# Kernel optimization log

Hardware: AMD Instinct MI355X
Metric: run time of the kernel (lower is better)

Reference implementation:

```python
import jax, jax.numpy as jnp
import numpy as np
from jax import lax

ALPHA = 0.1
B, C_IN, T, D_MODEL = 32, 512, 2048, 1024


def setup_inputs() -> dict:
    key = jax.random.key(0)
    k_x, k_w, k_b = jax.random.split(key, 3)
    x = jax.random.normal(k_x, (B, C_IN, T), dtype=jnp.float32)
    # nn.Linear(c_in, d_model): weight [d_model, c_in], bias [d_model]
    bound = 1.0 / np.sqrt(C_IN)
    W = jax.random.uniform(k_w, (D_MODEL, C_IN), dtype=jnp.float32, minval=-bound, maxval=bound)
    b = jax.random.uniform(k_b, (D_MODEL,), dtype=jnp.float32, minval=-bound, maxval=bound)
    return {"x": x, "W": W, "b": b}


def _ewma_scan(xt):
    # xt: [T, B, C] time-major; f_0 = x_0, f_t = a*x_t + (1-a)*f_{t-1}
    def step(carry, xi):
        carry = ALPHA * xi + (1.0 - ALPHA) * carry
        return carry, carry
    _, ys = lax.scan(step, xt[0], xt[1:])
    return jnp.concatenate([xt[:1], ys], axis=0)  # [T, B, C]


def reference(x, W, b):
    # x: [B, c_in, T] -> permute to [B, T, c_in]
    xp = jnp.transpose(x, (0, 2, 1))
    xt = jnp.moveaxis(xp, 1, 0)  # [T, B, c_in]
    fwd = _ewma_scan(xt)
    bwd = _ewma_scan(xt[::-1])[::-1]
    ewma = jnp.moveaxis((fwd + bwd) * 0.5, 0, 1)  # [B, T, c_in]
    # value embedding (dropout = identity at inference)
    return jnp.einsum('btc,dc->btd', ewma, W) + b
```

## Files before the change

### kernel.cpp

```cpp
#include <hip/hip_runtime.h>
#include <hip/hip_bf16.h>
#include <stdint.h>
#include <stddef.h>

#define T_LEN   2048
#define C_IN_   512
#define D_MODEL_ 1024
#define B_SZ    32

typedef __hip_bfloat16 bf16;
typedef __attribute__((ext_vector_type(8))) short short8;
typedef __attribute__((ext_vector_type(4))) float f32x4;

__device__ __forceinline__ void gload16(const void* g, void* l) {
    __builtin_amdgcn_global_load_lds(
        (const __attribute__((address_space(1))) uint32_t*)g,
        (__attribute__((address_space(3))) uint32_t*)l, 16, 0, 0);
}

__global__ void wconv_kernel(const float* __restrict__ W, bf16* __restrict__ Wb) {
    int i = blockIdx.x * 256 + threadIdx.x;
    float4 v = ((const float4*)W)[i];
    bf16* o = Wb + (size_t)i * 4;
    o[0] = __float2bfloat16(v.x);
    o[1] = __float2bfloat16(v.y);
    o[2] = __float2bfloat16(v.z);
    o[3] = __float2bfloat16(v.w);
}

__global__ __launch_bounds__(512)
void ewma_kernel(const float* __restrict__ x, bf16* __restrict__ A) {
    const int tid  = threadIdx.x;
    const int wid  = tid >> 6;
    const int lane = tid & 63;
    const int half = lane >> 5;
    const int j    = lane & 31;
    const int b    = blockIdx.x >> 5;
    const int cg   = blockIdx.x & 31;
    const int c_local = (wid << 1) | half;
    const int c    = (cg << 4) + c_local;

    const float AL = 0.1f, OM = 0.9f;
    const float Q  = 1.179018457773862e-3f;

    float xr[64];
    const float4* xp = (const float4*)(x + (size_t)(b * C_IN_ + c) * T_LEN + j * 64);
    #pragma unroll
    for (int i = 0; i < 16; ++i) {
        float4 v = xp[i];
        xr[4*i+0] = v.x; xr[4*i+1] = v.y; xr[4*i+2] = v.z; xr[4*i+3] = v.w;
    }

    float g = (j == 0) ? xr[0] : AL * xr[0];
    #pragma unroll
    for (int i = 1; i < 64; ++i) g = fmaf(OM, g, AL * xr[i]);

    float F = g, coef = Q;
    #pragma unroll
    for (int d = 1; d < 32; d <<= 1) {
        float up = __shfl_up(F, d, 32);
        F += (j >= d) ? coef * up : 0.0f;
        coef *= coef;
    }
    float carry = __shfl_up(F, 1, 32);
    if (j == 0) carry = 0.0f;

    xr[0] = (j == 0) ? xr[0] : fmaf(OM, carry, AL * xr[0]);
    #pragma unroll
    for (int i = 1; i < 64; ++i) xr[i] = fmaf(OM, xr[i-1], AL * xr[i]);

    float h;
    {
        float incL = xr[63] - OM * xr[62];
        if (j == 31) incL *= 10.0f;
        h = incL;
        #pragma unroll
        for (int i = 62; i >= 1; --i) h = fmaf(OM, h, xr[i] - OM * xr[i-1]);
        float inc0 = (j == 0) ? AL * xr[0] : (xr[0] - OM * carry);
        h = fmaf(OM, h, inc0);
    }

    float Bv = h; coef = Q;
    #pragma unroll
    for (int d = 1; d < 32; d <<= 1) {
        float dn = __shfl_down(Bv, d, 32);
        Bv += (j < 32 - d) ? coef * dn : 0.0f;
        coef *= coef;
    }
    float bnext = __shfl_down(Bv, 1, 32);
    if (j == 31) bnext = 0.0f;

    {
        float bp = bnext;
        float incL = xr[63] - OM * xr[62];
        if (j == 31) incL *= 10.0f;
        float bb = fmaf(OM, bp, incL);
        xr[63] = 0.5f * (xr[63] + bb);
        bp = bb;
        #pragma unroll
        for (int i = 62; i >= 1; --i) {
            float inc = xr[i] - OM * xr[i-1];
            bb = fmaf(OM, bp, inc);
            xr[i] = 0.5f * (xr[i] + bb);
            bp = bb;
        }
        float inc0 = (j == 0) ? AL * xr[0] : (xr[0] - OM * carry);
        bb = fmaf(OM, bp, inc0);
        xr[0] = 0.5f * (xr[0] + bb);
    }

    __shared__ bf16 stg[32 * 16 * 16];
    const size_t outbase = (size_t)(b * T_LEN) * C_IN_ + (cg << 4);
    #pragma unroll
    for (int grp = 0; grp < 4; ++grp) {
        __syncthreads();
        #pragma unroll
        for (int ii = 0; ii < 16; ++ii) {
            int elem = ((j * 16 + ii) * 16 + c_local) ^ ((j & 7) << 3);
            stg[elem] = __float2bfloat16(xr[grp * 16 + ii]);
        }
        __syncthreads();
        #pragma unroll
        for (int r = 0; r < 2; ++r) {
            int u   = tid * 2 + r;
            int jj  = u >> 5;
            int ii  = (u >> 1) & 15;
            int hf  = u & 1;
            int elem = ((jj * 16 + ii) * 16 + hf * 8) ^ ((jj & 7) << 3);
            float4 v = *(const float4*)&stg[elem];
            int t = jj * 64 + grp * 16 + ii;
            *(float4*)(A + outbase + (size_t)t * C_IN_ + hf * 8) = v;
        }
    }
}

#define MFMA(a, b, c) __builtin_amdgcn_mfma_f32_16x16x32_bf16(a, b, c, 0, 0, 0)

__global__ __launch_bounds__(512)
void gemm_kernel(const bf16* __restrict__ Amat, const bf16* __restrict__ Wb,
                 const float* __restrict__ bias, float* __restrict__ out) {
    constexpr int K = C_IN_, N = D_MODEL_;
    extern __shared__ bf16 lds[];
    const int tid  = threadIdx.x;
    const int wid  = tid >> 6, lane = tid & 63;
    const int wr   = wid >> 2, wc = wid & 3;
    const int lr   = lane & 15;
    const int lg   = lane >> 4;

    int bid = blockIdx.x;
    int swz = (bid & 7) * 128 + (bid >> 3);
    const int mb = swz >> 2, nb = swz & 3;
    const int m0 = mb * 256, n0 = nb * 256;

    auto base = [&](int s, int op, int hf) -> bf16* {
        return lds + (((s * 2 + op) * 2 + hf) << 13);
    };
    auto stage = [&](const bf16* g, int row0, int kt, int s, int op, int hf) {
        bf16* lb = base(s, op, hf);
        #pragma unroll
        for (int r = 0; r < 2; ++r) {
            int q = tid + r * 512;
            int row = q >> 3, u = q & 7;
            gload16(g + (size_t)(row0 + row) * K + kt * 64 + ((u ^ (row & 7)) << 3),
                    (char*)lb + q * 16);
        }
    };
    auto rdA = [&](int s, int mf, int ks) -> short8 {
        int row = mf * 16 + lr;
        int u   = ks * 4 + lg;
        return *(const short8*)((const char*)base(s, 0, wr)
                                + row * 128 + ((u ^ (row & 7)) << 4));
    };
    auto rdB = [&](int s, int nf, int ks) -> short8 {
        int row = (wc & 1) * 64 + nf * 16 + lr;
        int u   = ks * 4 + lg;
        return *(const short8*)((const char*)base(s, 1, wc >> 1)
                                + row * 128 + ((u ^ (row & 7)) << 4));
    };

    f32x4 acc[8][4];
    #pragma unroll
    for (int m = 0; m < 8; ++m)
        #pragma unroll
        for (int n = 0; n < 4; ++n) acc[m][n] = (f32x4){0.f, 0.f, 0.f, 0.f};

    stage(Amat, m0 + 0,   0, 0, 0, 0);
    stage(Amat, m0 + 128, 0, 0, 0, 1);
    stage(Wb,   n0 + 0,   0, 0, 1, 0);
    stage(Wb,   n0 + 128, 0, 0, 1, 1);
    stage(Amat, m0 + 0,   1, 1, 0, 0);
    asm volatile("s_waitcnt vmcnt(2)" ::: "memory");
    __builtin_amdgcn_s_barrier();

    #pragma unroll
    for (int kt = 0; kt < 8; ++kt) {
        const int s = kt & 1;
        short8 a[4][2], bA[2][2], bB[2][2];

        #pragma unroll
        for (int m = 0; m < 4; ++m) { a[m][0] = rdA(s, m, 0); a[m][1] = rdA(s, m, 1); }
        #pragma unroll
        for (int n = 0; n < 2; ++n) { bA[n][0] = rdB(s, n, 0); bA[n][1] = rdB(s, n, 1); }
        if (kt < 7) stage(Amat, m0 + 128, kt + 1, s ^ 1, 0, 1);
        __builtin_amdgcn_s_barrier();
        asm volatile("s_waitcnt lgkmcnt(0)");
        __builtin_amdgcn_sched_barrier(0);
        __builtin_amdgcn_s_setprio(1);
        #pragma unroll
        for (int m = 0; m < 4; ++m)
            #pragma unroll
            for (int n = 0; n < 2; ++n) {
                acc[m][n] = MFMA(a[m][0], bA[n][0], acc[m][n]);
                acc[m][n] = MFMA(a[m][1], bA[n][1], acc[m][n]);
            }
        __builtin_amdgcn_s_setprio(0);
        __builtin_amdgcn_s_barrier();

        #pragma unroll
        for (int n = 0; n < 2; ++n) { bB[n][0] = rdB(s, 2 + n, 0); bB[n][1] = rdB(s, 2 + n, 1); }
        if (kt < 7) stage(Wb, n0 + 0, kt + 1, s ^ 1, 1, 0);
        __builtin_amdgcn_s_barrier();
        asm volatile("s_waitcnt lgkmcnt(0)");
        __builtin_amdgcn_sched_barrier(0);
        __builtin_amdgcn_s_setprio(1);
        #pragma unroll
        for (int m = 0; m < 4; ++m)
            #pragma unroll
            for (int n = 0; n < 2; ++n) {
                acc[m][2 + n] = MFMA(a[m][0], bB[n][0], acc[m][2 + n]);
                acc[m][2 + n] = MFMA(a[m][1], bB[n][1], acc[m][2 + n]);
            }
        __builtin_amdgcn_s_setprio(0);
        __builtin_amdgcn_s_barrier();

        #pragma unroll
        for (int m = 0; m < 4; ++m) { a[m][0] = rdA(s, 4 + m, 0); a[m][1] = rdA(s, 4 + m, 1); }
        if (kt < 7) stage(Wb, n0 + 128, kt + 1, s ^ 1, 1, 1);
        __builtin_amdgcn_s_barrier();
        asm volatile("s_waitcnt lgkmcnt(0)");
        __builtin_amdgcn_sched_barrier(0);
        __builtin_amdgcn_s_setprio(1);
        #pragma unroll
        for (int m = 0; m < 4; ++m)
            #pragma unroll
            for (int n = 0; n < 2; ++n) {
                acc[4 + m][2 + n] = MFMA(a[m][0], bB[n][0], acc[4 + m][2 + n]);
                acc[4 + m][2 + n] = MFMA(a[m][1], bB[n][1], acc[4 + m][2 + n]);
            }
        __builtin_amdgcn_s_setprio(0);
        __builtin_amdgcn_s_barrier();

        if (kt < 6) stage(Amat, m0 + 0, kt + 2, s, 0, 0);
        __builtin_amdgcn_s_setprio(1);
        #pragma unroll
        for (int m = 0; m < 4; ++m)
            #pragma unroll
            for (int n = 0; n < 2; ++n) {
                acc[4 + m][n] = MFMA(a[m][0], bA[n][0], acc[4 + m][n]);
                acc[4 + m][n] = MFMA(a[m][1], bA[n][1], acc[4 + m][n]);
            }
        __builtin_amdgcn_s_setprio(0);
        if (kt < 6)       asm volatile("s_waitcnt vmcnt(2)" ::: "memory");
        else if (kt == 6) asm volatile("s_waitcnt vmcnt(0)" ::: "memory");
        __builtin_amdgcn_s_barrier();
    }

    const int crow = (lane >> 4) << 2;
    #pragma unroll
    for (int nf = 0; nf < 4; ++nf) {
        int col = n0 + wc * 64 + nf * 16 + lr;
        float bv = bias[col];
        #pragma unroll
        for (int mf = 0; mf < 8; ++mf) {
            size_t rbase = (size_t)(m0 + wr * 128 + mf * 16 + crow) * N + col;
            #pragma unroll
            for (int r = 0; r < 4; ++r)
                out[rbase + (size_t)r * N] = acc[mf][nf][r] + bv;
        }
    }
}

extern "C" void kernel_launch(void* const* d_in, const int* in_sizes, int n_in,
                              void* d_out, int out_size, void* d_ws, size_t ws_size,
                              hipStream_t stream) {
    const float* x    = (const float*)d_in[0];
    const float* W    = (const float*)d_in[1];
    const float* bias = (const float*)d_in[2];
    float* out = (float*)d_out;

    bf16* Wb   = (bf16*)d_ws;
    bf16* Amat = (bf16*)((char*)d_ws + (1 << 21));

    hipLaunchKernelGGL(wconv_kernel, dim3(512), dim3(256), 0, stream, W, Wb);
    hipLaunchKernelGGL(ewma_kernel, dim3(B_SZ * 32), dim3(512), 0, stream, x, Amat);
    hipLaunchKernelGGL(gemm_kernel,
                       dim3((B_SZ * T_LEN / 256) * (D_MODEL_ / 256)),
                       dim3(512), 131072, stream, Amat, Wb, bias, out);
}
```

Measured before the change: 172.6 us.

## Coalesce EWMA input loads through LDS and deepen GEMM prefetch schedule

The EWMA kernel now stages each block's 16 channel rows through shared memory with asynchronous global-to-LDS loads and a swizzle, instead of having each thread read its 64-element strided chunk directly. This targets coalescing of the input reads, at the cost of 64KB of LDS per block and extra barriers. The GEMM main loop is unrolled by two k-steps with a reordered staging sequence that keeps more loads in flight (vmcnt(4) instead of vmcnt(2)). It also drops the sched_barrier hints, which aims to hide global-load latency better but leaves instruction ordering to the compiler.

```diff
diff --git a/kernel.cpp b/kernel.cpp
--- a/kernel.cpp
+++ b/kernel.cpp
@@ -38,17 +38,36 @@
     const int b    = blockIdx.x >> 5;
     const int cg   = blockIdx.x & 31;
     const int c_local = (wid << 1) | half;
-    const int c    = (cg << 4) + c_local;
 
     const float AL = 0.1f, OM = 0.9f;
     const float Q  = 1.179018457773862e-3f;
 
+    __shared__ float buf[8 * 2048];
+    __shared__ bf16  stg[32 * 16 * 16];
+
     float xr[64];
-    const float4* xp = (const float4*)(x + (size_t)(b * C_IN_ + c) * T_LEN + j * 64);
-    #pragma unroll
-    for (int i = 0; i < 16; ++i) {
-        float4 v = xp[i];
-        xr[4*i+0] = v.x; xr[4*i+1] = v.y; xr[4*i+2] = v.z; xr[4*i+3] = v.w;
+    const size_t xbase = ((size_t)b * C_IN_ + (cg << 4)) * T_LEN;
+    const int srcu = tid ^ ((tid >> 4) & 7);
+
+    #pragma unroll
+    for (int h = 0; h < 2; ++h) {
+        #pragma unroll
+        for (int it = 0; it < 8; ++it)
+            gload16(x + xbase + (size_t)(h * 8 + it) * T_LEN + srcu * 4,
+                    (char*)buf + it * 8192 + tid * 16);
+        asm volatile("s_waitcnt vmcnt(0)" ::: "memory");
+        __syncthreads();
+        if ((c_local >> 3) == h) {
+            const char* rbase = (const char*)buf + (c_local & 7) * 8192;
+            #pragma unroll
+            for (int i = 0; i < 16; ++i) {
+                int p = (j * 16 + i) ^ (j & 7);
+                float4 v = *(const float4*)(rbase + p * 16);
+                xr[4*i+0] = v.x; xr[4*i+1] = v.y;
+                xr[4*i+2] = v.z; xr[4*i+3] = v.w;
+            }
+        }
+        __syncthreads();
     }
 
     float g = (j == 0) ? xr[0] : AL * xr[0];
@@ -69,18 +88,18 @@
     #pragma unroll
     for (int i = 1; i < 64; ++i) xr[i] = fmaf(OM, xr[i-1], AL * xr[i]);
 
-    float h;
+    float h2;
     {
         float incL = xr[63] - OM * xr[62];
         if (j == 31) incL *= 10.0f;
-        h = incL;
-        #pragma unroll
-        for (int i = 62; i >= 1; --i) h = fmaf(OM, h, xr[i] - OM * xr[i-1]);
+        h2 = incL;
+        #pragma unroll
+        for (int i = 62; i >= 1; --i) h2 = fmaf(OM, h2, xr[i] - OM * xr[i-1]);
         float inc0 = (j == 0) ? AL * xr[0] : (xr[0] - OM * carry);
-        h = fmaf(OM, h, inc0);
-    }
-
-    float Bv = h; coef = Q;
+        h2 = fmaf(OM, h2, inc0);
+    }
+
+    float Bv = h2; coef = Q;
     #pragma unroll
     for (int d = 1; d < 32; d <<= 1) {
         float dn = __shfl_down(Bv, d, 32);
@@ -109,7 +128,6 @@
         xr[0] = 0.5f * (xr[0] + bb);
     }
 
-    __shared__ bf16 stg[32 * 16 * 16];
     const size_t outbase = (size_t)(b * T_LEN) * C_IN_ + (cg << 4);
     #pragma unroll
     for (int grp = 0; grp < 4; ++grp) {
@@ -155,27 +173,27 @@
     auto base = [&](int s, int op, int hf) -> bf16* {
         return lds + (((s * 2 + op) * 2 + hf) << 13);
     };
-    auto stage = [&](const bf16* g, int row0, int kt, int s, int op, int hf) {
+    auto stageH = [&](int op, int hf, int kt, int s) {
+        const bf16* g = (op == 0) ? Amat + (size_t)(m0 + hf * 128) * K
+                                  : Wb   + (size_t)(n0 + hf * 128) * K;
         bf16* lb = base(s, op, hf);
         #pragma unroll
         for (int r = 0; r < 2; ++r) {
             int q = tid + r * 512;
             int row = q >> 3, u = q & 7;
-            gload16(g + (size_t)(row0 + row) * K + kt * 64 + ((u ^ (row & 7)) << 3),
+            gload16(g + (size_t)row * K + kt * 64 + ((u ^ (row & 7)) << 3),
                     (char*)lb + q * 16);
         }
     };
     auto rdA = [&](int s, int mf, int ks) -> short8 {
         int row = mf * 16 + lr;
-        int u   = ks * 4 + lg;
         return *(const short8*)((const char*)base(s, 0, wr)
-                                + row * 128 + ((u ^ (row & 7)) << 4));
+                                + row * 128 + (((ks * 4 + lg) ^ (row & 7)) << 4));
     };
     auto rdB = [&](int s, int nf, int ks) -> short8 {
         int row = (wc & 1) * 64 + nf * 16 + lr;
-        int u   = ks * 4 + lg;
         return *(const short8*)((const char*)base(s, 1, wc >> 1)
-                                + row * 128 + ((u ^ (row & 7)) << 4));
+                                + row * 128 + (((ks * 4 + lg) ^ (row & 7)) << 4));
     };
 
     f32x4 acc[8][4];
@@ -184,27 +202,23 @@
         #pragma unroll
         for (int n = 0; n < 4; ++n) acc[m][n] = (f32x4){0.f, 0.f, 0.f, 0.f};
 
-    stage(Amat, m0 + 0,   0, 0, 0, 0);
-    stage(Amat, m0 + 128, 0, 0, 0, 1);
-    stage(Wb,   n0 + 0,   0, 0, 1, 0);
-    stage(Wb,   n0 + 128, 0, 0, 1, 1);
-    stage(Amat, m0 + 0,   1, 1, 0, 0);
-    asm volatile("s_waitcnt vmcnt(2)" ::: "memory");
+    stageH(0, 0, 0, 0); stageH(0, 1, 0, 0); stageH(1, 0, 0, 0); stageH(1, 1, 0, 0);
+    stageH(1, 0, 1, 1); stageH(0, 0, 1, 1);
+    asm volatile("s_waitcnt vmcnt(4)" ::: "memory");
     __builtin_amdgcn_s_barrier();
 
     #pragma unroll
-    for (int kt = 0; kt < 8; ++kt) {
-        const int s = kt & 1;
+    for (int it = 0; it < 4; ++it) {
+        const int k0 = 2 * it;
         short8 a[4][2], bA[2][2], bB[2][2];
 
         #pragma unroll
-        for (int m = 0; m < 4; ++m) { a[m][0] = rdA(s, m, 0); a[m][1] = rdA(s, m, 1); }
-        #pragma unroll
-        for (int n = 0; n < 2; ++n) { bA[n][0] = rdB(s, n, 0); bA[n][1] = rdB(s, n, 1); }
-        if (kt < 7) stage(Amat, m0 + 128, kt + 1, s ^ 1, 0, 1);
-        __builtin_amdgcn_s_barrier();
-        asm volatile("s_waitcnt lgkmcnt(0)");
-        __builtin_amdgcn_sched_barrier(0);
+        for (int m = 0; m < 4; ++m) { a[m][0] = rdA(0, m, 0); a[m][1] = rdA(0, m, 1); }
+        #pragma unroll
+        for (int n = 0; n < 2; ++n) { bA[n][0] = rdB(0, n, 0); bA[n][1] = rdB(0, n, 1); }
+        stageH(0, 1, k0 + 1, 1);
+        __builtin_amdgcn_s_barrier();
+        asm volatile("s_waitcnt lgkmcnt(0)");
         __builtin_amdgcn_s_setprio(1);
         #pragma unroll
         for (int m = 0; m < 4; ++m)
@@ -217,11 +231,10 @@
         __builtin_amdgcn_s_barrier();
 
         #pragma unroll
-        for (int n = 0; n < 2; ++n) { bB[n][0] = rdB(s, 2 + n, 0); bB[n][1] = rdB(s, 2 + n, 1); }
-        if (kt < 7) stage(Wb, n0 + 0, kt + 1, s ^ 1, 1, 0);
-        __builtin_amdgcn_s_barrier();
-        asm volatile("s_waitcnt lgkmcnt(0)");
-        __builtin_amdgcn_sched_barrier(0);
+        for (int n = 0; n < 2; ++n) { bB[n][0] = rdB(0, 2 + n, 0); bB[n][1] = rdB(0, 2 + n, 1); }
+        stageH(1, 1, k0 + 1, 1);
+        __builtin_amdgcn_s_barrier();
+        asm volatile("s_waitcnt lgkmcnt(0)");
         __builtin_amdgcn_s_setprio(1);
         #pragma unroll
         for (int m = 0; m < 4; ++m)
@@ -234,11 +247,10 @@
         __builtin_amdgcn_s_barrier();
 
         #pragma unroll
-        for (int m = 0; m < 4; ++m) { a[m][0] = rdA(s, 4 + m, 0); a[m][1] = rdA(s, 4 + m, 1); }
-        if (kt < 7) stage(Wb, n0 + 128, kt + 1, s ^ 1, 1, 1);
-        __builtin_amdgcn_s_barrier();
-        asm volatile("s_waitcnt lgkmcnt(0)");
-        __builtin_amdgcn_sched_barrier(0);
+        for (int m = 0; m < 4; ++m) { a[m][0] = rdA(0, 4 + m, 0); a[m][1] = rdA(0, 4 + m, 1); }
+        if (it < 3) stageH(1, 0, k0 + 2, 0);
+        __builtin_amdgcn_s_barrier();
+        asm volatile("s_waitcnt lgkmcnt(0)");
         __builtin_amdgcn_s_setprio(1);
         #pragma unroll
         for (int m = 0; m < 4; ++m)
@@ -250,7 +262,7 @@
         __builtin_amdgcn_s_setprio(0);
         __builtin_amdgcn_s_barrier();
 
-        if (kt < 6) stage(Amat, m0 + 0, kt + 2, s, 0, 0);
+        if (it < 3) stageH(0, 0, k0 + 2, 0);
         __builtin_amdgcn_s_setprio(1);
         #pragma unroll
         for (int m = 0; m < 4; ++m)
@@ -260,8 +272,71 @@
                 acc[4 + m][n] = MFMA(a[m][1], bA[n][1], acc[4 + m][n]);
             }
         __builtin_amdgcn_s_setprio(0);
-        if (kt < 6)       asm volatile("s_waitcnt vmcnt(2)" ::: "memory");
-        else if (kt == 6) asm volatile("s_waitcnt vmcnt(0)" ::: "memory");
+        if (it < 3) asm volatile("s_waitcnt vmcnt(4)" ::: "memory");
+        else        asm volatile("s_waitcnt vmcnt(0)" ::: "memory");
+        __builtin_amdgcn_s_barrier();
+
+        #pragma unroll
+        for (int m = 0; m < 4; ++m) { a[m][0] = rdA(1, m, 0); a[m][1] = rdA(1, m, 1); }
+        #pragma unroll
+        for (int n = 0; n < 2; ++n) { bA[n][0] = rdB(1, n, 0); bA[n][1] = rdB(1, n, 1); }
+        if (it < 3) stageH(0, 1, k0 + 2, 0);
+        __builtin_amdgcn_s_barrier();
+        asm volatile("s_waitcnt lgkmcnt(0)");
+        __builtin_amdgcn_s_setprio(1);
+        #pragma unroll
+        for (int m = 0; m < 4; ++m)
+            #pragma unroll
+            for (int n = 0; n < 2; ++n) {
+                acc[m][n] = MFMA(a[m][0], bA[n][0], acc[m][n]);
+                acc[m][n] = MFMA(a[m][1], bA[n][1], acc[m][n]);
+            }
+        __builtin_amdgcn_s_setprio(0);
+        __builtin_amdgcn_s_barrier();
+
+        #pragma unroll
+        for (int n = 0; n < 2; ++n) { bB[n][0] = rdB(1, 2 + n, 0); bB[n][1] = rdB(1, 2 + n, 1); }
+        if (it < 3) stageH(1, 1, k0 + 2, 0);
+        __builtin_amdgcn_s_barrier();
+        asm volatile("s_waitcnt lgkmcnt(0)");
+        __builtin_amdgcn_s_setprio(1);
+        #pragma unroll
+        for (int m = 0; m < 4; ++m)
+            #pragma unroll
+            for (int n = 0; n < 2; ++n) {
+                acc[m][2 + n] = MFMA(a[m][0], bB[n][0], acc[m][2 + n]);
+                acc[m][2 + n] = MFMA(a[m][1], bB[n][1], acc[m][2 + n]);
+            }
+        __builtin_amdgcn_s_setprio(0);
+        __builtin_amdgcn_s_barrier();
+
+        #pragma unroll
+        for (int m = 0; m < 4; ++m) { a[m][0] = rdA(1, 4 + m, 0); a[m][1] = rdA(1, 4 + m, 1); }
+        if (it < 3) stageH(1, 0, k0 + 3, 1);
+        __builtin_amdgcn_s_barrier();
+        asm volatile("s_waitcnt lgkmcnt(0)");
+        __builtin_amdgcn_s_setprio(1);
+        #pragma unroll
+        for (int m = 0; m < 4; ++m)
+            #pragma unroll
+            for (int n = 0; n < 2; ++n) {
+                acc[4 + m][2 + n] = MFMA(a[m][0], bB[n][0], acc[4 + m][2 + n]);
+                acc[4 + m][2 + n] = MFMA(a[m][1], bB[n][1], acc[4 + m][2 + n]);
+            }
+        __builtin_amdgcn_s_setprio(0);
+        __builtin_amdgcn_s_barrier();
+
+        if (it < 3) stageH(0, 0, k0 + 3, 1);
+        __builtin_amdgcn_s_setprio(1);
+        #pragma unroll
+        for (int m = 0; m < 4; ++m)
+            #pragma unroll
+            for (int n = 0; n < 2; ++n) {
+                acc[4 + m][n] = MFMA(a[m][0], bA[n][0], acc[4 + m][n]);
+                acc[4 + m][n] = MFMA(a[m][1], bA[n][1], acc[4 + m][n]);
+            }
+        __builtin_amdgcn_s_setprio(0);
+        if (it < 3) asm volatile("s_waitcnt vmcnt(4)" ::: "memory");
         __builtin_amdgcn_s_barrier();
     }
 
```

After: 170.9 us. Within noise of the previous version (-1.0%).
